# Kernel optimization log

Hardware: AMD Instinct MI355X
Metric: run time of the kernel (lower is better)

The kernel has to match this reference:

```python
import jax, jax.numpy as jnp
import numpy as np


def quat_to_rot(q):
    # q: [B, 4] = (x, y, z, w); same math as from_quaternion in the source.
    x, y, z, w = q[:, 0], q[:, 1], q[:, 2], q[:, 3]
    tx, ty, tz = 2.0 * x, 2.0 * y, 2.0 * z
    twx, twy, twz = tx * w, ty * w, tz * w
    txx, txy, txz = tx * x, ty * x, tz * x
    tyy, tyz, tzz = ty * y, tz * y, tz * z
    r = jnp.stack([1.0 - (tyy + tzz), txy - twz, txz + twy,
                   txy + twz, 1.0 - (txx + tzz), tyz - twx,
                   txz - twy, tyz + twx, 1.0 - (txx + tyy)], axis=-1)
    return r.reshape(-1, 3, 3)


def matrix_from_params(transfos):
    B, N = transfos.shape
    R = quat_to_rot(transfos[:, :4])
    if N == 10:
        S = jax.vmap(jnp.diag)(transfos[:, -3:])
    else:
        S = jnp.broadcast_to(jnp.eye(3, dtype=transfos.dtype), (B, 3, 3))
    SR = jnp.matmul(S, R)
    if N == 7:
        t = transfos[:, 4:7][..., None]
    else:
        t = jnp.zeros((B, 3, 1), transfos.dtype)
    return jnp.concatenate([SR, t], axis=2)  # [B, 3, 4]


def spatial_transformer_3d(img, transfos, min_ref_grid, max_ref_grid):
    B, H, W, D, C = img.shape  # ref_size_xyz = (W, H, D) per the source
    theta = matrix_from_params(transfos)  # [B, 3, 4]

    xs = jnp.linspace(min_ref_grid[0], max_ref_grid[0], W)
    ys = jnp.linspace(min_ref_grid[1], max_ref_grid[1], H)
    zs = jnp.linspace(min_ref_grid[2], max_ref_grid[2], D)
    mz, my, mx = jnp.meshgrid(zs, ys, xs, indexing='ij')  # (D, H, W), x fastest
    Nel = D * H * W
    grid = jnp.stack([mx.ravel(), my.ravel(), mz.ravel(),
                      jnp.ones(Nel, dtype=img.dtype)], axis=0)  # (4, Nel)
    pts = jnp.einsum('bij,jn->bin', theta, grid)  # (B, 3, Nel)

    Wf, Hf, Df = float(W), float(H), float(D)
    cx = (Wf - 1.0) / (max_ref_grid[0] - min_ref_grid[0])
    cy = (Hf - 1.0) / (max_ref_grid[1] - min_ref_grid[1])
    cz = (Df - 1.0) / (max_ref_grid[2] - min_ref_grid[2])
    ix = cx * pts[:, 0, :] - cx * min_ref_grid[0]
    iy = cy * pts[:, 1, :] - cy * min_ref_grid[1]
    iz = cz * pts[:, 2, :] - cz * min_ref_grid[2]

    # padding_mode in {'zeros','min'}: validity mask for out-of-grid points
    valid = ((ix >= 0.0) & (ix <= Wf - 1.0) &
             (iy >= 0.0) & (iy <= Hf - 1.0) &
             (iz >= 0.0) & (iz <= Df - 1.0)).astype(img.dtype)[..., None]  # (B, Nel, 1)

    ix0 = jnp.clip(jnp.floor(ix), 0.0, Wf - 1.0)
    iy0 = jnp.clip(jnp.floor(iy), 0.0, Hf - 1.0)
    iz0 = jnp.clip(jnp.floor(iz), 0.0, Df - 1.0)

    imf = img.reshape(B, H * W * D, C)
    acc = jnp.zeros((B, Nel, C), img.dtype)
    for ox in (0.0, 1.0):
        for oy in (0.0, 1.0):
            for oz in (0.0, 1.0):
                gx, gy, gz = ix0 + ox, iy0 + oy, iz0 + oz  # corner coords
                w = (jnp.clip(1.0 - jnp.abs(ix - gx), 0.0, 1.0) *
                     jnp.clip(1.0 - jnp.abs(iy - gy), 0.0, 1.0) *
                     jnp.clip(1.0 - jnp.abs(iz - gz), 0.0, 1.0))
                gxi = jnp.clip(gx, 0.0, Wf - 1.0).astype(jnp.int32)
                gyi = jnp.clip(gy, 0.0, Hf - 1.0).astype(jnp.int32)
                gzi = jnp.clip(gz, 0.0, Df - 1.0).astype(jnp.int32)
                lin = (gyi * W + gxi) * D + gzi  # row-major index into [H, W, D]
                v = jnp.take_along_axis(imf, lin[..., None], axis=1)  # (B, Nel, C)
                acc = acc + w[..., None] * v

    # padding_mode == 'min': fill out-of-grid voxels with the per-volume minimum
    fill = jnp.min(img, axis=(1, 2, 3, 4))[:, None, None]  # (B, 1, 1)
    out = valid * acc + (1.0 - valid) * fill
    # grid was flattened in (z, y, x) order with x fastest -> back to (H, W, D)
    out = out.reshape(B, D, H, W, C).transpose(0, 2, 3, 1, 4)
    return out


def setup_inputs() -> dict:
    key = jax.random.key(0)
    k1, k2 = jax.random.split(key)
    img = jax.random.normal(k1, (4, 160, 160, 160, 1), dtype=jnp.float32)
    transfos = jax.random.normal(k2, (4, 7), dtype=jnp.float32)
    return {"img": img, "transfos": transfos}


def reference(img, transfos):
    min_ref_grid = (-1.0, -1.0, -1.0)
    max_ref_grid = (1.0, 1.0, 1.0)
    return spatial_transformer_3d(img, transfos, min_ref_grid, max_ref_grid)
```

## Files before the change

### kernel.cpp

```cpp
#include <hip/hip_runtime.h>

#define HH 160
#define WW 160
#define DD 160
#define BB 4
#define NPB (HH * WW * DD / 4)
#define K1B 256

typedef float vfloat4 __attribute__((ext_vector_type(4)));

__global__ __launch_bounds__(256) void min_cst_kernel(const float4* __restrict__ img4,
                                                      const float* __restrict__ transfos,
                                                      float* __restrict__ partial,
                                                      double* __restrict__ cst) {
    const int b = blockIdx.y;
    const size_t base = (size_t)b * NPB;
    const int t0 = blockIdx.x * 256 + threadIdx.x;
    const int S = K1B * 256;

    float m = 3.4e38f;
    #pragma unroll
    for (int r = 0; r < 4; r++) {
        const int i0 = t0 + 4 * r * S;
        float4 v0 = img4[base + i0];
        float4 v1 = img4[base + i0 + S];
        float4 v2 = img4[base + i0 + 2 * S];
        float4 v3 = make_float4(3.4e38f, 3.4e38f, 3.4e38f, 3.4e38f);
        if (i0 + 3 * S < NPB) v3 = img4[base + i0 + 3 * S];
        m = fminf(m, fminf(fminf(v0.x, v0.y), fminf(v0.z, v0.w)));
        m = fminf(m, fminf(fminf(v1.x, v1.y), fminf(v1.z, v1.w)));
        m = fminf(m, fminf(fminf(v2.x, v2.y), fminf(v2.z, v2.w)));
        m = fminf(m, fminf(fminf(v3.x, v3.y), fminf(v3.z, v3.w)));
    }

    #pragma unroll
    for (int o = 32; o >= 1; o >>= 1) m = fminf(m, __shfl_down(m, o));
    __shared__ float s[4];
    const int lane = threadIdx.x & 63, wid = threadIdx.x >> 6;
    if (lane == 0) s[wid] = m;
    __syncthreads();
    if (threadIdx.x == 0) {
        partial[b * K1B + blockIdx.x] =
            fminf(fminf(s[0], s[1]), fminf(s[2], s[3]));
    }

    if (blockIdx.x == 0 && blockIdx.y == 0 && threadIdx.x < BB) {
        const int bb = threadIdx.x;
        const float* q = transfos + bb * 7;
        double x = q[0], y = q[1], z = q[2], w = q[3];
        double tx = 2.0 * x, ty = 2.0 * y, tz = 2.0 * z;
        double twx = tx * w, twy = ty * w, twz = tz * w;
        double txx = tx * x, txy = ty * x, txz = tz * x;
        double tyy = ty * y, tyz = tz * y, tzz = tz * z;
        double R[3][3] = {
            {1.0 - (tyy + tzz), txy - twz,         txz + twy},
            {txy + twz,         1.0 - (txx + tzz), tyz - twx},
            {txz - twy,         tyz + twx,         1.0 - (txx + tyy)}
        };
        double t[3] = {(double)q[4], (double)q[5], (double)q[6]};
        for (int r = 0; r < 3; r++) {
            cst[bb * 12 + r * 4 + 0] = R[r][0];
            cst[bb * 12 + r * 4 + 1] = R[r][1];
            cst[bb * 12 + r * 4 + 2] = R[r][2];
            cst[bb * 12 + r * 4 + 3] = 79.5 * (t[r] - R[r][0] - R[r][1] - R[r][2] + 1.0);
        }
    }
}

__global__ __launch_bounds__(256) void st3d_kernel(const float* __restrict__ img,
                                                   const double* __restrict__ cst,
                                                   const float* __restrict__ partial,
                                                   float* __restrict__ out) {
    const int b = blockIdx.z;
    const int y = blockIdx.y;

    __shared__ float sred[4];
    float pm = partial[b * K1B + threadIdx.x];
    #pragma unroll
    for (int o = 32; o >= 1; o >>= 1) pm = fminf(pm, __shfl_down(pm, o));
    if ((threadIdx.x & 63) == 0) sred[threadIdx.x >> 6] = pm;
    __syncthreads();
    const float fill = fminf(fminf(sred[0], sred[1]), fminf(sred[2], sred[3]));

    const int t = blockIdx.x * 256 + threadIdx.x;
    const int x = t / 40;
    const int zq = (t - 40 * x) * 4;

    const double* c = cst + b * 12;
    const double c2 = c[2], c6 = c[6], c10 = c[10];
    const double dx = (double)x, dy = (double)y, dz = (double)zq;
    double ixd = fma(c[0], dx, fma(c[1], dy, fma(c2, dz, c[3])));
    double iyd = fma(c[4], dx, fma(c[5], dy, fma(c6, dz, c[7])));
    double izd = fma(c[8], dx, fma(c[9], dy, fma(c10, dz, c[11])));

    const float* base = img + (size_t)b * (HH * WW * DD);

    vfloat4 r;
    #pragma unroll
    for (int k = 0; k < 4; k++) {
        float res = fill;
        const bool valid = (ixd >= 0.0) && (ixd <= 159.0) && (iyd >= 0.0) &&
                           (iyd <= 159.0) && (izd >= 0.0) && (izd <= 159.0);
        if (valid) {
            double flx = floor(ixd), fly = floor(iyd), flz = floor(izd);
            int x0 = (int)flx, y0 = (int)fly, z0 = (int)flz;
            float fx = (float)(ixd - flx), fy = (float)(iyd - fly), fz = (float)(izd - flz);
            int x1 = min(x0 + 1, 159), y1 = min(y0 + 1, 159), z1 = min(z0 + 1, 159);
            const float* p00 = base + ((size_t)y0 * WW + x0) * DD;
            const float* p01 = base + ((size_t)y0 * WW + x1) * DD;
            const float* p10 = base + ((size_t)y1 * WW + x0) * DD;
            const float* p11 = base + ((size_t)y1 * WW + x1) * DD;
            float v000 = p00[z0], v001 = p00[z1];
            float v010 = p10[z0], v011 = p10[z1];
            float v100 = p01[z0], v101 = p01[z1];
            float v110 = p11[z0], v111 = p11[z1];
            float wx0 = 1.0f - fx, wx1 = fx;
            float wy0 = 1.0f - fy, wy1 = fy;
            float wz0 = 1.0f - fz, wz1 = fz;
            float acc;
            acc  = ((wx0 * wy0) * wz0) * v000;
            acc += ((wx0 * wy0) * wz1) * v001;
            acc += ((wx0 * wy1) * wz0) * v010;
            acc += ((wx0 * wy1) * wz1) * v011;
            acc += ((wx1 * wy0) * wz0) * v100;
            acc += ((wx1 * wy0) * wz1) * v101;
            acc += ((wx1 * wy1) * wz0) * v110;
            acc += ((wx1 * wy1) * wz1) * v111;
            res = acc;
        }
        r[k] = res;
        ixd += c2; iyd += c6; izd += c10;
    }

    vfloat4* outp = (vfloat4*)(out + (size_t)(b * HH + y) * (WW * DD) + x * DD + zq);
    __builtin_nontemporal_store(r, outp);
}

extern "C" void kernel_launch(void* const* d_in, const int* in_sizes, int n_in,
                              void* d_out, int out_size, void* d_ws, size_t ws_size,
                              hipStream_t stream) {
    const float* img = (const float*)d_in[0];
    const float* transfos = (const float*)d_in[1];
    float* out = (float*)d_out;
    float* partial = (float*)d_ws;
    double* cst = (double*)((char*)d_ws + 4096);

    min_cst_kernel<<<dim3(K1B, BB), 256, 0, stream>>>((const float4*)img, transfos,
                                                      partial, cst);
    st3d_kernel<<<dim3(25, 160, BB), 256, 0, stream>>>(img, cst, partial, out);
}
```

Measured before the change: 131.5 us.

## Tile output into 3D blocks and branch-free wave-uniform gather path

Each block now covers an 8x8 tile of (x,y) with 16 z values instead of a 1D strip along one y row. A rotated sampling footprint then touches a compact region of the source volume, which should improve cache locality for the gathers. Inside a wave, the per-lane validity branch is replaced by a wave-level any() test. Lanes in a wave that has any valid point compute with clamped indices and select fill afterwards, and whole waves that are out of range skip the loads. The cost is extra clamping and some wasted loads by invalid lanes that sit in mixed waves.

```diff
diff --git a/kernel.cpp b/kernel.cpp
--- a/kernel.cpp
+++ b/kernel.cpp
@@ -71,8 +71,9 @@
                                                    const double* __restrict__ cst,
                                                    const float* __restrict__ partial,
                                                    float* __restrict__ out) {
-    const int b = blockIdx.z;
-    const int y = blockIdx.y;
+    const int bzc = blockIdx.z;
+    const int b = bzc / 20;
+    const int yt = bzc - b * 20;
 
     __shared__ float sred[4];
     float pm = partial[b * K1B + threadIdx.x];
@@ -82,9 +83,13 @@
     __syncthreads();
     const float fill = fminf(fminf(sred[0], sred[1]), fminf(sred[2], sred[3]));
 
-    const int t = blockIdx.x * 256 + threadIdx.x;
-    const int x = t / 40;
-    const int zq = (t - 40 * x) * 4;
+    const int tz = threadIdx.x & 3;
+    const int tx = (threadIdx.x >> 2) & 7;
+    const int ty = threadIdx.x >> 5;
+
+    const int x  = blockIdx.y * 8 + tx;
+    const int y  = yt * 8 + ty;
+    const int zq = blockIdx.x * 16 + tz * 4;
 
     const double* c = cst + b * 12;
     const double c2 = c[2], c6 = c[6], c10 = c[10];
@@ -93,27 +98,40 @@
     double iyd = fma(c[4], dx, fma(c[5], dy, fma(c6, dz, c[7])));
     double izd = fma(c[8], dx, fma(c[9], dy, fma(c10, dz, c[11])));
 
+    bool anyv = false;
+    {
+        double ax = ixd, ay = iyd, az = izd;
+        #pragma unroll
+        for (int k = 0; k < 4; k++) {
+            anyv = anyv || ((ax >= 0.0) && (ax <= 159.0) && (ay >= 0.0) &&
+                            (ay <= 159.0) && (az >= 0.0) && (az <= 159.0));
+            ax += c2; ay += c6; az += c10;
+        }
+    }
+
     const float* base = img + (size_t)b * (HH * WW * DD);
+    vfloat4 r;
 
-    vfloat4 r;
-    #pragma unroll
-    for (int k = 0; k < 4; k++) {
-        float res = fill;
-        const bool valid = (ixd >= 0.0) && (ixd <= 159.0) && (iyd >= 0.0) &&
-                           (iyd <= 159.0) && (izd >= 0.0) && (izd <= 159.0);
-        if (valid) {
+    if (__any(anyv)) {
+        #pragma unroll
+        for (int k = 0; k < 4; k++) {
+            const bool valid = (ixd >= 0.0) && (ixd <= 159.0) && (iyd >= 0.0) &&
+                               (iyd <= 159.0) && (izd >= 0.0) && (izd <= 159.0);
             double flx = floor(ixd), fly = floor(iyd), flz = floor(izd);
             int x0 = (int)flx, y0 = (int)fly, z0 = (int)flz;
+            x0 = min(max(x0, 0), 159);
+            y0 = min(max(y0, 0), 159);
+            z0 = min(max(z0, 0), 159);
             float fx = (float)(ixd - flx), fy = (float)(iyd - fly), fz = (float)(izd - flz);
             int x1 = min(x0 + 1, 159), y1 = min(y0 + 1, 159), z1 = min(z0 + 1, 159);
-            const float* p00 = base + ((size_t)y0 * WW + x0) * DD;
-            const float* p01 = base + ((size_t)y0 * WW + x1) * DD;
-            const float* p10 = base + ((size_t)y1 * WW + x0) * DD;
-            const float* p11 = base + ((size_t)y1 * WW + x1) * DD;
-            float v000 = p00[z0], v001 = p00[z1];
-            float v010 = p10[z0], v011 = p10[z1];
-            float v100 = p01[z0], v101 = p01[z1];
-            float v110 = p11[z0], v111 = p11[z1];
+            const int o00 = (y0 * WW + x0) * DD;
+            const int o01 = (y0 * WW + x1) * DD;
+            const int o10 = (y1 * WW + x0) * DD;
+            const int o11 = (y1 * WW + x1) * DD;
+            float v000 = base[o00 + z0], v001 = base[o00 + z1];
+            float v010 = base[o10 + z0], v011 = base[o10 + z1];
+            float v100 = base[o01 + z0], v101 = base[o01 + z1];
+            float v110 = base[o11 + z0], v111 = base[o11 + z1];
             float wx0 = 1.0f - fx, wx1 = fx;
             float wy0 = 1.0f - fy, wy1 = fy;
             float wz0 = 1.0f - fz, wz1 = fz;
@@ -126,13 +144,14 @@
             acc += ((wx1 * wy0) * wz1) * v101;
             acc += ((wx1 * wy1) * wz0) * v110;
             acc += ((wx1 * wy1) * wz1) * v111;
-            res = acc;
+            r[k] = valid ? acc : fill;
+            ixd += c2; iyd += c6; izd += c10;
         }
-        r[k] = res;
-        ixd += c2; iyd += c6; izd += c10;
+    } else {
+        r[0] = fill; r[1] = fill; r[2] = fill; r[3] = fill;
     }
 
-    vfloat4* outp = (vfloat4*)(out + (size_t)(b * HH + y) * (WW * DD) + x * DD + zq);
+    vfloat4* outp = (vfloat4*)(out + (size_t)((b * HH + y) * WW + x) * DD + zq);
     __builtin_nontemporal_store(r, outp);
 }
 
@@ -147,5 +166,6 @@
 
     min_cst_kernel<<<dim3(K1B, BB), 256, 0, stream>>>((const float4*)img, transfos,
                                                       partial, cst);
-    st3d_kernel<<<dim3(25, 160, BB), 256, 0, stream>>>(img, cst, partial, out);
+    st3d_kernel<<<dim3(DD / 16, WW / 8, (HH / 8) * BB), 256, 0, stream>>>(img, cst,
+                                                                          partial, out);
 }
```

Measured after the change: 137.8 us. 1.05x slower.
